# Optimization experiments

Measured on AMD Instinct MI355X. Metric: run time of the kernel, lower is better.

## Reference

```python
import jax, jax.numpy as jnp
import numpy as np


def _hausdorff(x, y):
    # x, y: [B, C, N, D] point sets per (batch, channel); rows are points.
    x2 = jnp.sum(x * x, axis=-1)                       # [B, C, N]
    y2 = jnp.sum(y * y, axis=-1)                       # [B, C, M]
    xy = jnp.einsum('bcnd,bcmd->bcnm', x, y)           # [B, C, N, M]
    d2 = x2[..., :, None] + y2[..., None, :] - 2.0 * xy
    d = jnp.sqrt(jnp.maximum(d2, 0.0))                 # Euclidean distances
    d_fwd = jnp.max(jnp.min(d, axis=-1), axis=-1)      # max_n min_m, [B, C]
    d_bwd = jnp.max(jnp.min(d, axis=-2), axis=-1)      # max_m min_n, [B, C]
    return jnp.maximum(d_fwd, d_bwd)                   # symmetric Hausdorff [B, C]


def setup_inputs() -> dict:
    key = jax.random.key(0)
    k1, k2 = jax.random.split(key)
    B, C, H, W = 8, 3, 1024, 1024
    inp = jax.random.normal(k1, (B, C, H, W), dtype=jnp.float32)
    tgt = jax.random.normal(k2, (B, C, H, W), dtype=jnp.float32)
    return {'input': inp, 'target': tgt}


def reference(input, target):
    h = _hausdorff(input, target)        # [B, C]
    # original: sum_i mean_c(h[i]) / B == mean over (B, C)
    return jnp.mean(h)
```

## Files before the change

kernel.cpp:

```cpp
#include <hip/hip_runtime.h>
#include <math.h>

constexpr int BC = 24;
constexpr int N  = 1024;
constexpr int D  = 1024;
constexpr int TILE = 128;
constexpr int SKF = 40;

typedef short short8 __attribute__((ext_vector_type(8)));
typedef float f32x4  __attribute__((ext_vector_type(4)));
typedef long lng2    __attribute__((ext_vector_type(2)));

#define FINF 3.402823466e+38f


__device__ inline unsigned pk_bf16(float a, float b) {
    unsigned ua = __float_as_uint(a) + 0x8000u;
    unsigned ub = __float_as_uint(b) + 0x8000u;
    return __builtin_amdgcn_perm(ub, ua, 0x07060302);
}

__device__ inline int pk_fp8x4(float a, float b, float c, float d) {
    int w = __builtin_amdgcn_cvt_pk_fp8_f32(a, b, 0, false);
    w = __builtin_amdgcn_cvt_pk_fp8_f32(c, d, w, true);
    return w;
}

__global__ __launch_bounds__(256) void prep_kernel(const float* __restrict__ X,
                                                   const float* __restrict__ Y,
                                                   unsigned char* __restrict__ Xf8,
                                                   unsigned char* __restrict__ Yf8,
                                                   float* __restrict__ xn,
                                                   float* __restrict__ yn,
                                                   unsigned* __restrict__ clr,
                                                   unsigned* __restrict__ outc) {
    if (threadIdx.x < 16) clr[blockIdx.x * 16 + threadIdx.x] = 0xFFFFFFFFu;
    if (blockIdx.x == 0 && threadIdx.x == 16) *outc = 0u;

    __shared__ unsigned lds[16 * 260];
    int wave = threadIdx.x >> 6, lane = threadIdx.x & 63;
    int gid = blockIdx.x;
    bool isY = gid >= 1536;
    int g = isY ? gid - 1536 : gid;
    int bc = g >> 6, R = g & 63;

    const float* __restrict__ src = (isY ? Y : X)
        + ((size_t)bc * N + (size_t)R * 16 + wave * 4) * D + lane * 4;
    unsigned char* __restrict__ dst = (isY ? Yf8 : Xf8)
        + (size_t)(bc * 64 + R) * 16384;
    float* __restrict__ nrm = (isY ? yn : xn) + bc * N + R * 16 + wave * 4;

    float4 v[4][4];
    #pragma unroll
    for (int i = 0; i < 4; i++)
        #pragma unroll
        for (int q = 0; q < 4; q++)
            v[i][q] = *(const float4*)(src + (size_t)i * D + q * 256);

    float4 ns;
    float* nsp = (float*)&ns;
    #pragma unroll
    for (int i = 0; i < 4; i++) {
        int r = wave * 4 + i;
        float s = 0.f;
        #pragma unroll
        for (int q = 0; q < 4; q++) {
            float4 c = v[i][q];
            lds[r * 260 + q * 64 + lane] = (unsigned)pk_fp8x4(c.x, c.y, c.z, c.w);
            s += c.x * c.x + c.y * c.y + c.z * c.z + c.w * c.w;
        }
        #pragma unroll
        for (int m = 1; m < 64; m <<= 1) s += __shfl_xor(s, m, 64);
        nsp[i] = s;
    }
    if (lane == 0) *(float4*)nrm = ns;

    __syncthreads();

    int r16 = lane & 15, quad = lane >> 4;
    #pragma unroll
    for (int gr = 0; gr < 4; gr++) {
        int Kp = gr * 4 + wave;
        int di = r16 * 260 + Kp * 16 + quad * 2;
        uint2 d0 = *(const uint2*)&lds[di];
        uint2 d1 = *(const uint2*)&lds[di + 8];
        uint4 w4 = make_uint4(d0.x, d0.y, d1.x, d1.y);
        *(uint4*)(dst + Kp * 1024 + quad * 256 + r16 * 16) = w4;
    }
}

__global__ __launch_bounds__(256, 3) void tile_f8_kernel(const unsigned char* __restrict__ Xf8,
                                                         const unsigned char* __restrict__ Yf8,
                                                         const float* __restrict__ xn,
                                                         const float* __restrict__ yn,
                                                         unsigned* __restrict__ rowmin,
                                                         unsigned* __restrict__ colmin,
                                                         float* __restrict__ out) {
    __shared__ float wred[4][4];
    __shared__ int lastflag;

    int raw = blockIdx.x;
    int id = (raw & 7) * 192 + (raw >> 3);
    int bc = id >> 6;
    int tn = (id >> 3) & 7, tm = id & 7;

    int wave = threadIdx.x >> 6, lane = threadIdx.x & 63;
    int wr = wave >> 1, wc = wave & 1;
    int quad = lane >> 4, tx = lane & 15;

    const unsigned char* Xb = Xf8 + (size_t)bc * 1024 * 1024;
    const unsigned char* Yb = Yf8 + (size_t)bc * 1024 * 1024;
    const unsigned char* ax = Xb + (size_t)(tn * 8 + wr * 4) * 16 * 1024 + lane * 16;
    const unsigned char* by = Yb + (size_t)(tm * 8 + wc * 4) * 16 * 1024 + lane * 16;

    f32x4 acc[4][4];
    #pragma unroll
    for (int i = 0; i < 4; i++)
        #pragma unroll
        for (int j = 0; j < 4; j++) acc[i][j] = (f32x4)0.f;

    lng2 a[2][4], b[2][4];
    #pragma unroll
    for (int mi = 0; mi < 4; mi++) {
        a[0][mi] = *(const lng2*)(ax + mi * 16384);
        b[0][mi] = *(const lng2*)(by + mi * 16384);
    }
    #pragma unroll
    for (int Kp = 0; Kp < 16; Kp++) {
        int cur = Kp & 1, nxt = cur ^ 1;
        if (Kp < 15) {
            #pragma unroll
            for (int mi = 0; mi < 4; mi++) {
                a[nxt][mi] = *(const lng2*)(ax + mi * 16384 + (Kp + 1) * 1024);
                b[nxt][mi] = *(const lng2*)(by + mi * 16384 + (Kp + 1) * 1024);
            }
        }
        #pragma unroll
        for (int mi = 0; mi < 4; mi++)
            #pragma unroll
            for (int mj = 0; mj < 4; mj++)
                acc[mi][mj] = __builtin_amdgcn_mfma_f32_16x16x32_fp8_fp8(a[cur][mi].x, b[cur][mj].x, acc[mi][mj], 0, 0, 0);
        #pragma unroll
        for (int mi = 0; mi < 4; mi++)
            #pragma unroll
            for (int mj = 0; mj < 4; mj++)
                acc[mi][mj] = __builtin_amdgcn_mfma_f32_16x16x32_fp8_fp8(a[cur][mi].y, b[cur][mj].y, acc[mi][mj], 0, 0, 0);
    }

    int rbase = bc * N + tn * TILE + wr * 64;
    int cbase = bc * N + tm * TILE + wc * 64;
    float xnr[4][4], ynr[4];
    #pragma unroll
    for (int mi = 0; mi < 4; mi++)
        #pragma unroll
        for (int r = 0; r < 4; r++) xnr[mi][r] = xn[rbase + mi * 16 + quad * 4 + r];
    #pragma unroll
    for (int mj = 0; mj < 4; mj++) ynr[mj] = yn[cbase + mj * 16 + tx];

    float rmin[4][4], cmin[4];
    #pragma unroll
    for (int mi = 0; mi < 4; mi++)
        #pragma unroll
        for (int r = 0; r < 4; r++) rmin[mi][r] = FINF;
    #pragma unroll
    for (int mj = 0; mj < 4; mj++) cmin[mj] = FINF;

    #pragma unroll
    for (int mi = 0; mi < 4; mi++)
        #pragma unroll
        for (int mj = 0; mj < 4; mj++)
            #pragma unroll
            for (int r = 0; r < 4; r++) {
                float d2 = fmaxf(xnr[mi][r] + ynr[mj] - 2.f * acc[mi][mj][r], 0.f);
                rmin[mi][r] = fminf(rmin[mi][r], d2);
                cmin[mj]    = fminf(cmin[mj], d2);
            }

    #pragma unroll
    for (int m = 1; m < 16; m <<= 1)
        #pragma unroll
        for (int mi = 0; mi < 4; mi++)
            #pragma unroll
            for (int r = 0; r < 4; r++)
                rmin[mi][r] = fminf(rmin[mi][r], __shfl_xor(rmin[mi][r], m, 64));
    if (tx == 0) {
        #pragma unroll
        for (int mi = 0; mi < 4; mi++)
            #pragma unroll
            for (int r = 0; r < 4; r++)
                atomicMin(&rowmin[rbase + mi * 16 + quad * 4 + r], __float_as_uint(rmin[mi][r]));
    }
    #pragma unroll
    for (int m = 16; m < 64; m <<= 1)
        #pragma unroll
        for (int mj = 0; mj < 4; mj++)
            cmin[mj] = fminf(cmin[mj], __shfl_xor(cmin[mj], m, 64));
    if (quad == 0) {
        #pragma unroll
        for (int mj = 0; mj < 4; mj++)
            atomicMin(&colmin[cbase + mj * 16 + tx], __float_as_uint(cmin[mj]));
    }

    asm volatile("s_waitcnt vmcnt(0)" ::: "memory");
    __syncthreads();
    if (threadIdx.x == 0) {
        unsigned t = atomicAdd((unsigned*)out, 1u);
        lastflag = (t == 1535u);
    }
    __syncthreads();
    if (lastflag) {
        float acc_sum = 0.f;
        #pragma unroll 1
        for (int grp = 0; grp < 6; grp++) {
            float bmax[4];
            #pragma unroll
            for (int c = 0; c < 4; c++) bmax[c] = 0.f;
            #pragma unroll
            for (int c = 0; c < 4; c++) {
                int base = (grp * 4 + c) * N;
                #pragma unroll
                for (int q = 0; q < 4; q++) {
                    unsigned ur = __hip_atomic_load(&rowmin[base + q * 256 + threadIdx.x],
                                                    __ATOMIC_RELAXED, __HIP_MEMORY_SCOPE_AGENT);
                    unsigned uc = __hip_atomic_load(&colmin[base + q * 256 + threadIdx.x],
                                                    __ATOMIC_RELAXED, __HIP_MEMORY_SCOPE_AGENT);
                    bmax[c] = fmaxf(bmax[c],
                                    fmaxf(__uint_as_float(ur), __uint_as_float(uc)));
                }
            }
            #pragma unroll
            for (int c = 0; c < 4; c++)
                #pragma unroll
                for (int m = 1; m < 64; m <<= 1)
                    bmax[c] = fmaxf(bmax[c], __shfl_xor(bmax[c], m, 64));
            if (lane == 0) {
                #pragma unroll
                for (int c = 0; c < 4; c++) wred[wave][c] = bmax[c];
            }
            __syncthreads();
            if (threadIdx.x == 0) {
                #pragma unroll
                for (int c = 0; c < 4; c++) {
                    float mx = fmaxf(fmaxf(wred[0][c], wred[1][c]),
                                     fmaxf(wred[2][c], wred[3][c]));
                    acc_sum += sqrtf(mx);
                }
            }
            __syncthreads();
        }
        if (threadIdx.x == 0) *out = acc_sum * (1.0f / (float)BC);
    }
}

__global__ __launch_bounds__(256) void norms_kernel(const float* __restrict__ X,
                                                    const float* __restrict__ Y,
                                                    float* __restrict__ xn,
                                                    float* __restrict__ yn) {
    int w = threadIdx.x >> 6, lane = threadIdx.x & 63;
    long rid = (long)blockIdx.x * 4 + w;
    bool isY = rid >= (long)BC * N;
    long row = isY ? rid - (long)BC * N : rid;
    const float* src = (isY ? Y : X) + row * D;
    float s = 0.f;
    #pragma unroll
    for (int q = 0; q < 4; q++) {
        float4 v = ((const float4*)src)[lane + q * 64];
        s += v.x * v.x + v.y * v.y + v.z * v.z + v.w * v.w;
    }
    #pragma unroll
    for (int m = 1; m < 64; m <<= 1) s += __shfl_xor(s, m, 64);
    if (lane == 0) (isY ? yn : xn)[row] = s;
}

__global__ __launch_bounds__(256) void tile_conv_kernel(const float* __restrict__ X,
                                                        const float* __restrict__ Y,
                                                        const float* __restrict__ xn,
                                                        const float* __restrict__ yn,
                                                        unsigned* __restrict__ rowmin,
                                                        unsigned* __restrict__ colmin) {
    __shared__ unsigned short Xs[TILE * SKF];
    __shared__ unsigned short Ys[TILE * SKF];
    int bc = blockIdx.z, tn = blockIdx.y, tm = blockIdx.x;
    const float* Xb = X + ((size_t)bc * N + (size_t)tn * TILE) * D;
    const float* Yb = Y + ((size_t)bc * N + (size_t)tm * TILE) * D;

    int t = threadIdx.x;
    int srow = t >> 3, sq = t & 7;
    int wave = t >> 6, lane = t & 63;
    int wr = wave >> 1, wc = wave & 1;
    int quad = lane >> 4, tx = lane & 15;

    f32x4 acc[4][4];
    #pragma unroll
    for (int i = 0; i < 4; i++)
        #pragma unroll
        for (int j = 0; j < 4; j++) acc[i][j] = (f32x4)0.f;

    float4 xv[4], yv[4];
    #pragma unroll
    for (int i = 0; i < 4; i++) {
        xv[i] = *(const float4*)(Xb + (size_t)(srow + i * 32) * D + sq * 4);
        yv[i] = *(const float4*)(Yb + (size_t)(srow + i * 32) * D + sq * 4);
    }

    for (int k0 = 0; k0 < D; k0 += 32) {
        __syncthreads();
        #pragma unroll
        for (int i = 0; i < 4; i++) {
            uint2 px; px.x = pk_bf16(xv[i].x, xv[i].y); px.y = pk_bf16(xv[i].z, xv[i].w);
            *(uint2*)&Xs[(srow + i * 32) * SKF + sq * 4] = px;
            uint2 py; py.x = pk_bf16(yv[i].x, yv[i].y); py.y = pk_bf16(yv[i].z, yv[i].w);
            *(uint2*)&Ys[(srow + i * 32) * SKF + sq * 4] = py;
        }
        __syncthreads();
        if (k0 + 32 < D) {
            #pragma unroll
            for (int i = 0; i < 4; i++) {
                xv[i] = *(const float4*)(Xb + (size_t)(srow + i * 32) * D + k0 + 32 + sq * 4);
                yv[i] = *(const float4*)(Yb + (size_t)(srow + i * 32) * D + k0 + 32 + sq * 4);
            }
        }
        short8 af[4], bg[4];
        #pragma unroll
        for (int mi = 0; mi < 4; mi++)
            af[mi] = *(const short8*)&Xs[(wr * 64 + mi * 16 + tx) * SKF + quad * 8];
        #pragma unroll
        for (int mj = 0; mj < 4; mj++)
            bg[mj] = *(const short8*)&Ys[(wc * 64 + mj * 16 + tx) * SKF + quad * 8];
        #pragma unroll
        for (int mi = 0; mi < 4; mi++)
            #pragma unroll
            for (int mj = 0; mj < 4; mj++)
                acc[mi][mj] = __builtin_amdgcn_mfma_f32_16x16x32_bf16(af[mi], bg[mj], acc[mi][mj], 0, 0, 0);
    }

    int rbase = bc * N + tn * TILE + wr * 64;
    int cbase = bc * N + tm * TILE + wc * 64;
    float xnr[4][4], ynr[4];
    #pragma unroll
    for (int mi = 0; mi < 4; mi++)
        #pragma unroll
        for (int r = 0; r < 4; r++) xnr[mi][r] = xn[rbase + mi * 16 + quad * 4 + r];
    #pragma unroll
    for (int mj = 0; mj < 4; mj++) ynr[mj] = yn[cbase + mj * 16 + tx];

    float rmin[4][4], cmin[4];
    #pragma unroll
    for (int mi = 0; mi < 4; mi++)
        #pragma unroll
        for (int r = 0; r < 4; r++) rmin[mi][r] = FINF;
    #pragma unroll
    for (int mj = 0; mj < 4; mj++) cmin[mj] = FINF;

    #pragma unroll
    for (int mi = 0; mi < 4; mi++)
        #pragma unroll
        for (int mj = 0; mj < 4; mj++)
            #pragma unroll
            for (int r = 0; r < 4; r++) {
                float d2 = fmaxf(xnr[mi][r] + ynr[mj] - 2.f * acc[mi][mj][r], 0.f);
                rmin[mi][r] = fminf(rmin[mi][r], d2);
                cmin[mj]    = fminf(cmin[mj], d2);
            }

    #pragma unroll
    for (int m = 1; m < 16; m <<= 1)
        #pragma unroll
        for (int mi = 0; mi < 4; mi++)
            #pragma unroll
            for (int r = 0; r < 4; r++)
                rmin[mi][r] = fminf(rmin[mi][r], __shfl_xor(rmin[mi][r], m, 64));
    if (tx == 0) {
        #pragma unroll
        for (int mi = 0; mi < 4; mi++)
            #pragma unroll
            for (int r = 0; r < 4; r++)
                atomicMin(&rowmin[rbase + mi * 16 + quad * 4 + r], __float_as_uint(rmin[mi][r]));
    }
    #pragma unroll
    for (int m = 16; m < 64; m <<= 1)
        #pragma unroll
        for (int mj = 0; mj < 4; mj++)
            cmin[mj] = fminf(cmin[mj], __shfl_xor(cmin[mj], m, 64));
    if (quad == 0) {
        #pragma unroll
        for (int mj = 0; mj < 4; mj++)
            atomicMin(&colmin[cbase + mj * 16 + tx], __float_as_uint(cmin[mj]));
    }
}

__global__ __launch_bounds__(256) void finalize_kernel(const unsigned* __restrict__ rowmin,
                                                       const unsigned* __restrict__ colmin,
                                                       float* __restrict__ out) {
    int bc = blockIdx.x;
    float v = 0.f;
    for (int i = threadIdx.x; i < N; i += 256) {
        v = fmaxf(v, __uint_as_float(rowmin[bc * N + i]));
        v = fmaxf(v, __uint_as_float(colmin[bc * N + i]));
    }
    #pragma unroll
    for (int m = 1; m < 64; m <<= 1) v = fmaxf(v, __shfl_xor(v, m, 64));
    __shared__ float ws[4];
    int lane = threadIdx.x & 63, w = threadIdx.x >> 6;
    if (lane == 0) ws[w] = v;
    __syncthreads();
    if (threadIdx.x == 0) {
        float m = fmaxf(fmaxf(ws[0], ws[1]), fmaxf(ws[2], ws[3]));
        atomicAdd(out, sqrtf(m) * (1.0f / (float)BC));
    }
}

extern "C" void kernel_launch(void* const* d_in, const int* in_sizes, int n_in,
                              void* d_out, int out_size, void* d_ws, size_t ws_size,
                              hipStream_t stream) {
    const float* X = (const float*)d_in[0];
    const float* Y = (const float*)d_in[1];
    float* out = (float*)d_out;

    unsigned* rowmin = (unsigned*)d_ws;
    unsigned* colmin = rowmin + BC * N;
    float* xn = (float*)(colmin + BC * N);
    float* yn = xn + BC * N;
    size_t head = (size_t)4 * BC * N * 4;
    size_t f8_bytes = (size_t)BC * N * D;

    if (ws_size >= head + 2 * f8_bytes) {
        unsigned char* Xf8 = (unsigned char*)d_ws + head;
        unsigned char* Yf8 = Xf8 + f8_bytes;
        prep_kernel<<<3072, 256, 0, stream>>>(X, Y, Xf8, Yf8, xn, yn,
                                              rowmin, (unsigned*)out);
        tile_f8_kernel<<<1536, 256, 0, stream>>>(Xf8, Yf8, xn, yn,
                                                 rowmin, colmin, out);
    } else {
        hipMemsetAsync(d_ws, 0xFF, (size_t)2 * BC * N * 4, stream);
        hipMemsetAsync(d_out, 0, sizeof(float), stream);
        dim3 grid(N / TILE, N / TILE, BC);
        norms_kernel<<<2 * BC * N / 4, 256, 0, stream>>>(X, Y, xn, yn);
        tile_conv_kernel<<<grid, 256, 0, stream>>>(X, Y, xn, yn, rowmin, colmin);
        finalize_kernel<<<BC, 256, 0, stream>>>(rowmin, colmin, out);
    }
}
```

Before: 278.0 us.

## Stage fp32 rows into LDS via global_load_lds in prep kernel

Rewrites the prep kernel so fp32 input rows are copied straight into shared memory with buffer-to-LDS loads, in two halves of 8 rows, instead of going through registers. FP8 packing, the transpose write and the row-norm reduction now read from that LDS copy, and the norm is reduced across waves through a small shared array. The aim is to cut register pressure and get better load throughput in this memory-bound conversion pass. In exchange it adds extra barriers, a serial two-half loop and 8-byte global stores in place of 16-byte ones.

```diff
diff --git a/kernel.cpp b/kernel.cpp
--- a/kernel.cpp
+++ b/kernel.cpp
@@ -24,6 +24,13 @@
     int w = __builtin_amdgcn_cvt_pk_fp8_f32(a, b, 0, false);
     w = __builtin_amdgcn_cvt_pk_fp8_f32(c, d, w, true);
     return w;
+}
+
+__device__ inline void gll16(const float* g, void* l) {
+    __builtin_amdgcn_global_load_lds(
+        (const __attribute__((address_space(1))) unsigned*)g,
+        (__attribute__((address_space(3))) unsigned*)l,
+        16, 0, 0);
 }
 
 __global__ __launch_bounds__(256) void prep_kernel(const float* __restrict__ X,
@@ -34,58 +41,63 @@
                                                    float* __restrict__ yn,
                                                    unsigned* __restrict__ clr,
                                                    unsigned* __restrict__ outc) {
+    __shared__ unsigned ldsdw[8 * 1028];
+    __shared__ float npart[4][8];
+
     if (threadIdx.x < 16) clr[blockIdx.x * 16 + threadIdx.x] = 0xFFFFFFFFu;
     if (blockIdx.x == 0 && threadIdx.x == 16) *outc = 0u;
 
-    __shared__ unsigned lds[16 * 260];
     int wave = threadIdx.x >> 6, lane = threadIdx.x & 63;
     int gid = blockIdx.x;
     bool isY = gid >= 1536;
     int g = isY ? gid - 1536 : gid;
     int bc = g >> 6, R = g & 63;
 
-    const float* __restrict__ src = (isY ? Y : X)
-        + ((size_t)bc * N + (size_t)R * 16 + wave * 4) * D + lane * 4;
+    const float* __restrict__ srcb = (isY ? Y : X) + ((size_t)bc * N + (size_t)R * 16) * D;
     unsigned char* __restrict__ dst = (isY ? Yf8 : Xf8)
         + (size_t)(bc * 64 + R) * 16384;
-    float* __restrict__ nrm = (isY ? yn : xn) + bc * N + R * 16 + wave * 4;
-
-    float4 v[4][4];
-    #pragma unroll
-    for (int i = 0; i < 4; i++)
-        #pragma unroll
-        for (int q = 0; q < 4; q++)
-            v[i][q] = *(const float4*)(src + (size_t)i * D + q * 256);
-
-    float4 ns;
-    float* nsp = (float*)&ns;
-    #pragma unroll
-    for (int i = 0; i < 4; i++) {
-        int r = wave * 4 + i;
-        float s = 0.f;
-        #pragma unroll
-        for (int q = 0; q < 4; q++) {
-            float4 c = v[i][q];
-            lds[r * 260 + q * 64 + lane] = (unsigned)pk_fp8x4(c.x, c.y, c.z, c.w);
-            s += c.x * c.x + c.y * c.y + c.z * c.z + c.w * c.w;
-        }
-        #pragma unroll
-        for (int m = 1; m < 64; m <<= 1) s += __shfl_xor(s, m, 64);
-        nsp[i] = s;
-    }
-    if (lane == 0) *(float4*)nrm = ns;
-
-    __syncthreads();
-
-    int r16 = lane & 15, quad = lane >> 4;
-    #pragma unroll
-    for (int gr = 0; gr < 4; gr++) {
-        int Kp = gr * 4 + wave;
-        int di = r16 * 260 + Kp * 16 + quad * 2;
-        uint2 d0 = *(const uint2*)&lds[di];
-        uint2 d1 = *(const uint2*)&lds[di + 8];
-        uint4 w4 = make_uint4(d0.x, d0.y, d1.x, d1.y);
-        *(uint4*)(dst + Kp * 1024 + quad * 256 + r16 * 16) = w4;
+    float* __restrict__ nrm = (isY ? yn : xn) + bc * N + R * 16;
+
+    int r8 = lane & 7, g3 = lane >> 3;
+    int quad = g3 & 3, dose = g3 >> 2;
+
+    #pragma unroll 1
+    for (int h = 0; h < 2; h++) {
+        #pragma unroll
+        for (int rr = 0; rr < 2; rr++) {
+            int r = wave * 2 + rr;
+            const float* grow = srcb + (size_t)(h * 8 + r) * D + lane * 4;
+            char* lrow = (char*)&ldsdw[r * 1028];
+            #pragma unroll
+            for (int s = 0; s < 4; s++)
+                gll16(grow + s * 256, lrow + s * 1024);
+        }
+        asm volatile("s_waitcnt vmcnt(0)" ::: "memory");
+        __syncthreads();
+
+        float part = 0.f;
+        #pragma unroll
+        for (int kk = 0; kk < 4; kk++) {
+            int Kp = wave * 4 + kk;
+            const float* p = (const float*)&ldsdw[r8 * 1028 + Kp * 64 + dose * 32 + quad * 8];
+            float4 a = *(const float4*)p;
+            float4 b = *(const float4*)(p + 4);
+            uint2 w2;
+            w2.x = (unsigned)pk_fp8x4(a.x, a.y, a.z, a.w);
+            w2.y = (unsigned)pk_fp8x4(b.x, b.y, b.z, b.w);
+            *(uint2*)(dst + Kp * 1024 + quad * 256 + (h * 8 + r8) * 16 + dose * 8) = w2;
+            part += a.x * a.x + a.y * a.y + a.z * a.z + a.w * a.w
+                  + b.x * b.x + b.y * b.y + b.z * b.z + b.w * b.w;
+        }
+        part += __shfl_xor(part, 8, 64);
+        part += __shfl_xor(part, 16, 64);
+        part += __shfl_xor(part, 32, 64);
+        if (lane < 8) npart[wave][lane] = part;
+        __syncthreads();
+        if (wave == 0 && lane < 8)
+            nrm[h * 8 + lane] = npart[0][lane] + npart[1][lane]
+                              + npart[2][lane] + npart[3][lane];
+        __syncthreads();
     }
 }
 
```

New measurement: 280.6 us. Within noise of the previous version (+0.9%).
